# Performance work log

Hardware: AMD Instinct MI355X
Metric: run time of the kernel (lower is better)

Reference implementation:

```python
import jax, jax.numpy as jnp
import numpy as np

B, T, I, H, O = 256, 1024, 128, 256, 1

def setup_inputs() -> dict:
    key = jax.random.key(0)
    ks = jax.random.split(key, 7)
    s_ih = 1.0 / np.sqrt(H)
    return {
        "x": jax.random.normal(ks[0], (B, T, I), dtype=jnp.float32),
        "W_ih": jax.random.uniform(ks[1], (4 * H, I), minval=-s_ih, maxval=s_ih, dtype=jnp.float32),
        "W_hh": jax.random.uniform(ks[2], (4 * H, H), minval=-s_ih, maxval=s_ih, dtype=jnp.float32),
        "b_ih": jax.random.uniform(ks[3], (4 * H,), minval=-s_ih, maxval=s_ih, dtype=jnp.float32),
        "b_hh": jax.random.uniform(ks[4], (4 * H,), minval=-s_ih, maxval=s_ih, dtype=jnp.float32),
        "W_fc": jax.random.uniform(ks[5], (O, H), minval=-s_ih, maxval=s_ih, dtype=jnp.float32),
        "b_fc": jax.random.uniform(ks[6], (O,), minval=-s_ih, maxval=s_ih, dtype=jnp.float32),
    }

def _lstm_forward(x, W_ih, W_hh, b_ih, b_hh, W_fc, b_fc):
    # Precompute input projections for all timesteps in one big GEMM: [B,T,4H]
    x_proj = jnp.einsum('bti,gi->btg', x, W_ih) + b_ih + b_hh
    h0 = jnp.zeros((x.shape[0], W_hh.shape[1]), dtype=x.dtype)
    c0 = jnp.zeros_like(h0)
    Hd = W_hh.shape[1]

    def step(carry, xp_t):
        h, c = carry
        gates = xp_t + h @ W_hh.T  # [B, 4H]
        i_g = jax.nn.sigmoid(gates[:, 0 * Hd:1 * Hd])  # PyTorch gate order: i,f,g,o
        f_g = jax.nn.sigmoid(gates[:, 1 * Hd:2 * Hd])
        g_g = jnp.tanh(gates[:, 2 * Hd:3 * Hd])
        o_g = jax.nn.sigmoid(gates[:, 3 * Hd:4 * Hd])
        c_new = f_g * c + i_g * g_g
        h_new = o_g * jnp.tanh(c_new)
        return (h_new, c_new), None

    (h_T, _), _ = jax.lax.scan(step, (h0, c0), jnp.swapaxes(x_proj, 0, 1))
    return h_T @ W_fc.T + b_fc  # [B, O]

def reference(x, W_ih, W_hh, b_ih, b_hh, W_fc, b_fc):
    return _lstm_forward(x, W_ih, W_hh, b_ih, b_hh, W_fc, b_fc)
```

## Files before the change

### kernel.cpp

```cpp
#include <hip/hip_runtime.h>
#include <stdint.h>
#include <math.h>


typedef __attribute__((ext_vector_type(8))) __bf16 bf16x8;
typedef __attribute__((ext_vector_type(4))) float f32x4;
typedef __attribute__((ext_vector_type(4))) unsigned int u32x4;
typedef unsigned short u16;
typedef unsigned int u32;
typedef unsigned long long u64;

#define BK  16
#define JP  32
#define TT  1024
#define HD  256
#define ID  128

__device__ __forceinline__ u16 f2bf(float f) {
  u32 u = __float_as_uint(f);
  u += 0x7FFFu + ((u >> 16) & 1u);
  return (u16)(u >> 16);
}
__device__ __forceinline__ float bf2f(u16 h) { return __uint_as_float((u32)h << 16); }
__device__ __forceinline__ f32x4 mfma(bf16x8 a, bf16x8 b, f32x4 c) {
  return __builtin_amdgcn_mfma_f32_16x16x32_bf16(a, b, c, 0, 0, 0);
}
__device__ __forceinline__ float sigf(float x) {
  return __builtin_amdgcn_rcpf(1.f + __expf(-x));
}
__device__ __forceinline__ float tanhfast(float x) {
  float e = __expf(2.f * x);
  return 1.f - 2.f * __builtin_amdgcn_rcpf(e + 1.f);
}

__global__ __launch_bounds__(512, 2) void lstm_pk(
    const float* __restrict__ x, const float* __restrict__ Wih,
    const float* __restrict__ Whh, const float* __restrict__ bih,
    const float* __restrict__ bhh, const float* __restrict__ Wfc,
    const float* __restrict__ bfc, float* __restrict__ out,
    u16* __restrict__ hg)
{
  __shared__ u16 hHi[16][264], hLo[16][264];
  __shared__ u16 xHI[2][16][136], xLO[2][16][136];
  __shared__ u16 hS[2][2][16][40];
  __shared__ float red[8][16];

  const int tid  = threadIdx.x;
  const int bb   = blockIdx.x & 15, cb = blockIdx.x >> 4;
  const int b0   = bb * BK;
  const int lane = tid & 63, wave = tid >> 6;
  const int q    = lane >> 4, bcol = lane & 15;
  const int koff = q * 8;
  const int r15  = lane & 15;
  const int grow = (r15 & 3) * HD + cb * JP + wave * 4 + (r15 >> 2);
  const int jloc = wave * 4 + q;

  bf16x8 ahh_h[8], ahh_l[8], aih_h[4], aih_l[4];
#pragma unroll
  for (int kk = 0; kk < 8; ++kk) {
    const float* s = Whh + (size_t)grow * HD + kk * 32 + koff;
    float4 w0 = *(const float4*)(s), w1 = *(const float4*)(s + 4);
    float w[8] = {w0.x, w0.y, w0.z, w0.w, w1.x, w1.y, w1.z, w1.w};
    union { bf16x8 v; u16 u[8]; } th, tl;
#pragma unroll
    for (int e = 0; e < 8; ++e) {
      u16 hi = f2bf(w[e]); th.u[e] = hi; tl.u[e] = f2bf(w[e] - bf2f(hi));
    }
    ahh_h[kk] = th.v; ahh_l[kk] = tl.v;
  }
#pragma unroll
  for (int kk = 0; kk < 4; ++kk) {
    const float* s = Wih + (size_t)grow * ID + kk * 32 + koff;
    float4 w0 = *(const float4*)(s), w1 = *(const float4*)(s + 4);
    float w[8] = {w0.x, w0.y, w0.z, w0.w, w1.x, w1.y, w1.z, w1.w};
    union { bf16x8 v; u16 u[8]; } th, tl;
#pragma unroll
    for (int e = 0; e < 8; ++e) {
      u16 hi = f2bf(w[e]); th.u[e] = hi; tl.u[e] = f2bf(w[e] - bf2f(hi));
    }
    aih_h[kk] = th.v; aih_l[kk] = tl.v;
  }
  float biasr[4];
#pragma unroll
  for (int r = 0; r < 4; ++r) {
    int gr = r * HD + cb * JP + jloc;
    biasr[r] = bih[gr] + bhh[gr];
  }

  const int lb = tid >> 5;
  const int lc = (tid & 31) * 8;
  const u16* pH0 = hg + (((u32)(0 * 256 + b0 + lb)) << 8) + lc;
  const u16* pL0 = hg + (((u32)(1 * 256 + b0 + lb)) << 8) + lc;
  const u16* pH1 = hg + (((u32)(2 * 256 + b0 + lb)) << 8) + lc;
  const u16* pL1 = hg + (((u32)(3 * 256 + b0 + lb)) << 8) + lc;

  {
    int bi = tid >> 5, e4 = (tid & 31) * 4;
    float4 v = *(const float4*)(x + ((size_t)(b0 + bi) * TT) * ID + e4);
    float vf[4] = {v.x, v.y, v.z, v.w};
#pragma unroll
    for (int qq = 0; qq < 2; ++qq) {
      u16 h0 = f2bf(vf[2 * qq]),            h1 = f2bf(vf[2 * qq + 1]);
      u16 l0 = f2bf(vf[2 * qq] - bf2f(h0)), l1 = f2bf(vf[2 * qq + 1] - bf2f(h1));
      *(u32*)&xHI[0][bi][e4 + 2 * qq] = (u32)h0 | ((u32)h1 << 16);
      *(u32*)&xLO[0][bi][e4 + 2 * qq] = (u32)l0 | ((u32)l1 << 16);
    }
  }
  __syncthreads();

  float c_reg = 0.f, h_last = 0.f;

  for (int t = 0; t < TT; ++t) {
    const int p = t & 1, pn = p ^ 1;
    const u32 tag  = (u32)t & 3u;
    const u32 pat  = (tag & 1u) | ((tag >> 1) << 16);
    const u32 tagn = (u32)(t + 1) & 3u;
    const u16* aH = p ? pH1 : pH0;
    const u16* aL = p ? pL1 : pL0;

    u32x4 f0, f1;
    asm volatile("global_load_dwordx4 %0, %2, off sc0 sc1\n\t"
                 "global_load_dwordx4 %1, %3, off sc0 sc1"
                 : "=v"(f0), "=v"(f1) : "v"(aH), "v"(aL));

    f32x4 a0 = {0, 0, 0, 0}, a1 = {0, 0, 0, 0}, a2 = {0, 0, 0, 0};
#pragma unroll
    for (int kk = 0; kk < 4; ++kk) {
      bf16x8 bh = *(const bf16x8*)&xHI[p][bcol][kk * 32 + koff];
      bf16x8 bl = *(const bf16x8*)&xLO[p][bcol][kk * 32 + koff];
      a0 = mfma(aih_h[kk], bh, a0);
      a1 = mfma(aih_h[kk], bl, a1);
      a2 = mfma(aih_l[kk], bh, a2);
    }

    for (;;) {
      asm volatile("s_waitcnt vmcnt(0)" : "+v"(f0), "+v"(f1));
      u32 ok = (u32)((f0[0] & 0x10001u) == pat) & (u32)((f0[2] & 0x10001u) == pat)
             & (u32)((f1[0] & 0x10001u) == pat) & (u32)((f1[2] & 0x10001u) == pat);
      if (__all((int)ok)) break;
      __builtin_amdgcn_s_sleep(1);
      asm volatile("global_load_dwordx4 %0, %2, off sc0 sc1\n\t"
                   "global_load_dwordx4 %1, %3, off sc0 sc1\n\t"
                   "s_waitcnt vmcnt(0)"
                   : "=v"(f0), "=v"(f1) : "v"(aH), "v"(aL) : "memory");
    }

    float4 xv;
    if (t + 1 < TT)
      xv = *(const float4*)(x + ((size_t)(b0 + (tid >> 5)) * TT + (t + 1)) * ID + (tid & 31) * 4);

    *(u32x4*)&hHi[lb][lc] = f0;
    *(u32x4*)&hLo[lb][lc] = f1;
    __syncthreads();

#pragma unroll
    for (int kk = 0; kk < 8; ++kk) {
      bf16x8 bh = *(const bf16x8*)&hHi[bcol][kk * 32 + koff];
      bf16x8 bl = *(const bf16x8*)&hLo[bcol][kk * 32 + koff];
      a0 = mfma(ahh_h[kk], bh, a0);
      a1 = mfma(ahh_h[kk], bl, a1);
      a2 = mfma(ahh_l[kk], bh, a2);
    }

    {
      float g0 = a0[0] + a1[0] + a2[0] + biasr[0];
      float g1 = a0[1] + a1[1] + a2[1] + biasr[1];
      float g2 = a0[2] + a1[2] + a2[2] + biasr[2];
      float g3 = a0[3] + a1[3] + a2[3] + biasr[3];
      float ig = sigf(g0), fg = sigf(g1), gg = tanhfast(g2), og = sigf(g3);
      c_reg = fg * c_reg + ig * gg;
      float hn = og * tanhfast(c_reg);
      h_last = hn;
      u32 hi = f2bf(hn);
      if (q == 0) hi = (hi & ~1u) | (tagn & 1u);
      if (q == 1) hi = (hi & ~1u) | ((tagn >> 1) & 1u);
      u16 hi16 = (u16)hi;
      u32 lo = f2bf(hn - bf2f(hi16));
      if (q == 0) lo = (lo & ~1u) | (tagn & 1u);
      if (q == 1) lo = (lo & ~1u) | ((tagn >> 1) & 1u);
      hS[0][p][bcol][jloc] = hi16;
      hS[1][p][bcol][jloc] = (u16)lo;
    }

    if (t + 1 < TT) {
      float vf[4] = {xv.x, xv.y, xv.z, xv.w};
      int bi = tid >> 5, e4 = (tid & 31) * 4;
#pragma unroll
      for (int qq = 0; qq < 2; ++qq) {
        u16 h0 = f2bf(vf[2 * qq]),            h1 = f2bf(vf[2 * qq + 1]);
        u16 l0 = f2bf(vf[2 * qq] - bf2f(h0)), l1 = f2bf(vf[2 * qq + 1] - bf2f(h1));
        *(u32*)&xHI[pn][bi][e4 + 2 * qq] = (u32)h0 | ((u32)h1 << 16);
        *(u32*)&xLO[pn][bi][e4 + 2 * qq] = (u32)l0 | ((u32)l1 << 16);
      }
    }
    __syncthreads();

    if (tid >= 256) {
      int t2 = tid - 256, a = t2 >> 7, rem = t2 & 127, b = rem >> 3, ch = rem & 7;
      u64 v = *(const u64*)&hS[a][p][b][ch * 4];
      const u16* dst = hg + (((u32)((pn * 2 + a) * 256 + b0 + b)) << 8)
                          + (u32)(cb * JP + ch * 4);
      asm volatile("global_store_dwordx2 %0, %1, off sc0 sc1"
                   :: "v"(dst), "v"(v) : "memory");
    }
  }

  {
    float v = h_last * Wfc[cb * JP + jloc];
    v += __shfl_xor(v, 16);
    v += __shfl_xor(v, 32);
    if (lane < 16) red[wave][lane] = v;
  }
  __syncthreads();
  if (tid < 16) {
    float s = 0.f;
#pragma unroll
    for (int w = 0; w < 8; ++w) s += red[w][tid];
    if (cb == 0) s += bfc[0];
    atomicAdd(&out[b0 + tid], s);
  }
}

extern "C" void kernel_launch(void* const* d_in, const int* in_sizes, int n_in,
                              void* d_out, int out_size, void* d_ws, size_t ws_size,
                              hipStream_t stream) {
  const float* x   = (const float*)d_in[0];
  const float* Wih = (const float*)d_in[1];
  const float* Whh = (const float*)d_in[2];
  const float* bih = (const float*)d_in[3];
  const float* bhh = (const float*)d_in[4];
  const float* Wfc = (const float*)d_in[5];
  const float* bfc = (const float*)d_in[6];
  float* out = (float*)d_out;

  u16* hg = (u16*)d_ws;
  const size_t need = 4ull * 256 * 256 * sizeof(u16);

  hipMemsetAsync(d_ws, 0, need, stream);
  hipMemsetAsync(d_out, 0, (size_t)out_size * sizeof(float), stream);
  lstm_pk<<<128, 512, 0, stream>>>(x, Wih, Whh, bih, bhh, Wfc, bfc, out, hg);
}
```

Measured before the change: 2.736 ms.

## Interleave two batch groups per block to hide cross-block h exchange latency

Each block now handles two 16-row batch groups, A and B, over the same 32 hidden columns, and the grid is halved to 64 blocks. While group A's h-state poll and compute run, group B's global loads are already in flight, and the reverse. The aim is to overlap the inter-block synchronisation latency that dominates each timestep. Hi and lo bf16 halves are packed into one u32 per element and published directly per thread with a single store, replacing the shared staging area and the separate store phase. The risk is that half as many blocks leaves much of the GPU idle, and per-step serial work per block doubles.

```diff
diff --git a/kernel.cpp b/kernel.cpp
--- a/kernel.cpp
+++ b/kernel.cpp
@@ -8,9 +8,7 @@
 typedef __attribute__((ext_vector_type(4))) unsigned int u32x4;
 typedef unsigned short u16;
 typedef unsigned int u32;
-typedef unsigned long long u64;
-
-#define BK  16
+
 #define JP  32
 #define TT  1024
 #define HD  256
@@ -33,21 +31,20 @@
   return 1.f - 2.f * __builtin_amdgcn_rcpf(e + 1.f);
 }
 
-__global__ __launch_bounds__(512, 2) void lstm_pk(
+__global__ __launch_bounds__(512, 1) void lstm_pk(
     const float* __restrict__ x, const float* __restrict__ Wih,
     const float* __restrict__ Whh, const float* __restrict__ bih,
     const float* __restrict__ bhh, const float* __restrict__ Wfc,
     const float* __restrict__ bfc, float* __restrict__ out,
-    u16* __restrict__ hg)
+    u32* __restrict__ hg)
 {
-  __shared__ u16 hHi[16][264], hLo[16][264];
-  __shared__ u16 xHI[2][16][136], xLO[2][16][136];
-  __shared__ u16 hS[2][2][16][40];
+  __shared__ u16 hHi[2][16][264], hLo[2][16][264];
+  __shared__ u16 xHI[2][2][16][136], xLO[2][2][16][136];
   __shared__ float red[8][16];
 
   const int tid  = threadIdx.x;
-  const int bb   = blockIdx.x & 15, cb = blockIdx.x >> 4;
-  const int b0   = bb * BK;
+  const int pid  = blockIdx.x & 7, cb = blockIdx.x >> 3;
+  const int b0A  = pid * 16, b0B = (pid + 8) * 16;
   const int lane = tid & 63, wave = tid >> 6;
   const int q    = lane >> 4, bcol = lane & 15;
   const int koff = q * 8;
@@ -86,129 +83,167 @@
     int gr = r * HD + cb * JP + jloc;
     biasr[r] = bih[gr] + bhh[gr];
   }
-
-  const int lb = tid >> 5;
-  const int lc = (tid & 31) * 8;
-  const u16* pH0 = hg + (((u32)(0 * 256 + b0 + lb)) << 8) + lc;
-  const u16* pL0 = hg + (((u32)(1 * 256 + b0 + lb)) << 8) + lc;
-  const u16* pH1 = hg + (((u32)(2 * 256 + b0 + lb)) << 8) + lc;
-  const u16* pL1 = hg + (((u32)(3 * 256 + b0 + lb)) << 8) + lc;
-
-  {
-    int bi = tid >> 5, e4 = (tid & 31) * 4;
-    float4 v = *(const float4*)(x + ((size_t)(b0 + bi) * TT) * ID + e4);
-    float vf[4] = {v.x, v.y, v.z, v.w};
-#pragma unroll
-    for (int qq = 0; qq < 2; ++qq) {
-      u16 h0 = f2bf(vf[2 * qq]),            h1 = f2bf(vf[2 * qq + 1]);
-      u16 l0 = f2bf(vf[2 * qq] - bf2f(h0)), l1 = f2bf(vf[2 * qq + 1] - bf2f(h1));
-      *(u32*)&xHI[0][bi][e4 + 2 * qq] = (u32)h0 | ((u32)h1 << 16);
-      *(u32*)&xLO[0][bi][e4 + 2 * qq] = (u32)l0 | ((u32)l1 << 16);
-    }
-  }
-  __syncthreads();
-
-  float c_reg = 0.f, h_last = 0.f;
-
-  for (int t = 0; t < TT; ++t) {
-    const int p = t & 1, pn = p ^ 1;
-    const u32 tag  = (u32)t & 3u;
-    const u32 pat  = (tag & 1u) | ((tag >> 1) << 16);
-    const u32 tagn = (u32)(t + 1) & 3u;
-    const u16* aH = p ? pH1 : pH0;
-    const u16* aL = p ? pL1 : pL0;
-
-    u32x4 f0, f1;
+  float wfc = Wfc[cb * JP + jloc];
+  float bf0 = bfc[0];
+
+  const int lb = tid >> 5, lc = (tid & 31) * 8;
+  const u32* ldA0 = hg +           (b0A + lb) * 256 + lc;
+  const u32* ldA1 = hg + 65536 +   (b0A + lb) * 256 + lc;
+  const u32* ldB0 = hg +           (b0B + lb) * 256 + lc;
+  const u32* ldB1 = hg + 65536 +   (b0B + lb) * 256 + lc;
+  u32* pbA0 = hg +         (b0A + bcol) * 256 + cb * JP + jloc;
+  u32* pbA1 = pbA0 + 65536;
+  u32* pbB0 = hg +         (b0B + bcol) * 256 + cb * JP + jloc;
+  u32* pbB1 = pbB0 + 65536;
+  const float* xbA = x + (size_t)(b0A + lb) * TT * ID + (tid & 31) * 4;
+  const float* xbB = x + (size_t)(b0B + lb) * TT * ID + (tid & 31) * 4;
+
+  auto issue2 = [&](u32x4& g0, u32x4& g1, const u32* ap) {
     asm volatile("global_load_dwordx4 %0, %2, off sc0 sc1\n\t"
-                 "global_load_dwordx4 %1, %3, off sc0 sc1"
-                 : "=v"(f0), "=v"(f1) : "v"(aH), "v"(aL));
-
-    f32x4 a0 = {0, 0, 0, 0}, a1 = {0, 0, 0, 0}, a2 = {0, 0, 0, 0};
+                 "global_load_dwordx4 %1, %2, off offset:16 sc0 sc1"
+                 : "=v"(g0), "=v"(g1) : "v"(ap));
+  };
+  auto loadx = [&](f32x4& v, const float* ap) {
+    asm volatile("global_load_dwordx4 %0, %1, off" : "=v"(v) : "v"(ap));
+  };
+  auto pubst = [&](u32* ap, u32 w) {
+    asm volatile("global_store_dword %0, %1, off sc0 sc1" :: "v"(ap), "v"(w) : "memory");
+  };
+  auto xproj = [&](int g, int buf, f32x4& a0, f32x4& a1, f32x4& a2) {
 #pragma unroll
     for (int kk = 0; kk < 4; ++kk) {
-      bf16x8 bh = *(const bf16x8*)&xHI[p][bcol][kk * 32 + koff];
-      bf16x8 bl = *(const bf16x8*)&xLO[p][bcol][kk * 32 + koff];
+      bf16x8 bh = *(const bf16x8*)&xHI[g][buf][bcol][kk * 32 + koff];
+      bf16x8 bl = *(const bf16x8*)&xLO[g][buf][bcol][kk * 32 + koff];
       a0 = mfma(aih_h[kk], bh, a0);
       a1 = mfma(aih_h[kk], bl, a1);
       a2 = mfma(aih_l[kk], bh, a2);
     }
-
-    for (;;) {
-      asm volatile("s_waitcnt vmcnt(0)" : "+v"(f0), "+v"(f1));
-      u32 ok = (u32)((f0[0] & 0x10001u) == pat) & (u32)((f0[2] & 0x10001u) == pat)
-             & (u32)((f1[0] & 0x10001u) == pat) & (u32)((f1[2] & 0x10001u) == pat);
-      if (__all((int)ok)) break;
-      __builtin_amdgcn_s_sleep(1);
-      asm volatile("global_load_dwordx4 %0, %2, off sc0 sc1\n\t"
-                   "global_load_dwordx4 %1, %3, off sc0 sc1\n\t"
-                   "s_waitcnt vmcnt(0)"
-                   : "=v"(f0), "=v"(f1) : "v"(aH), "v"(aL) : "memory");
-    }
-
-    float4 xv;
-    if (t + 1 < TT)
-      xv = *(const float4*)(x + ((size_t)(b0 + (tid >> 5)) * TT + (t + 1)) * ID + (tid & 31) * 4);
-
-    *(u32x4*)&hHi[lb][lc] = f0;
-    *(u32x4*)&hLo[lb][lc] = f1;
-    __syncthreads();
-
+  };
+  auto hproj = [&](int g, f32x4& a0, f32x4& a1, f32x4& a2) {
 #pragma unroll
     for (int kk = 0; kk < 8; ++kk) {
-      bf16x8 bh = *(const bf16x8*)&hHi[bcol][kk * 32 + koff];
-      bf16x8 bl = *(const bf16x8*)&hLo[bcol][kk * 32 + koff];
+      bf16x8 bh = *(const bf16x8*)&hHi[g][bcol][kk * 32 + koff];
+      bf16x8 bl = *(const bf16x8*)&hLo[g][bcol][kk * 32 + koff];
       a0 = mfma(ahh_h[kk], bh, a0);
       a1 = mfma(ahh_h[kk], bl, a1);
       a2 = mfma(ahh_l[kk], bh, a2);
     }
-
-    {
-      float g0 = a0[0] + a1[0] + a2[0] + biasr[0];
-      float g1 = a0[1] + a1[1] + a2[1] + biasr[1];
-      float g2 = a0[2] + a1[2] + a2[2] + biasr[2];
-      float g3 = a0[3] + a1[3] + a2[3] + biasr[3];
-      float ig = sigf(g0), fg = sigf(g1), gg = tanhfast(g2), og = sigf(g3);
-      c_reg = fg * c_reg + ig * gg;
-      float hn = og * tanhfast(c_reg);
-      h_last = hn;
-      u32 hi = f2bf(hn);
-      if (q == 0) hi = (hi & ~1u) | (tagn & 1u);
-      if (q == 1) hi = (hi & ~1u) | ((tagn >> 1) & 1u);
-      u16 hi16 = (u16)hi;
-      u32 lo = f2bf(hn - bf2f(hi16));
-      if (q == 0) lo = (lo & ~1u) | (tagn & 1u);
-      if (q == 1) lo = (lo & ~1u) | ((tagn >> 1) & 1u);
-      hS[0][p][bcol][jloc] = hi16;
-      hS[1][p][bcol][jloc] = (u16)lo;
-    }
-
-    if (t + 1 < TT) {
-      float vf[4] = {xv.x, xv.y, xv.z, xv.w};
-      int bi = tid >> 5, e4 = (tid & 31) * 4;
-#pragma unroll
-      for (int qq = 0; qq < 2; ++qq) {
-        u16 h0 = f2bf(vf[2 * qq]),            h1 = f2bf(vf[2 * qq + 1]);
-        u16 l0 = f2bf(vf[2 * qq] - bf2f(h0)), l1 = f2bf(vf[2 * qq + 1] - bf2f(h1));
-        *(u32*)&xHI[pn][bi][e4 + 2 * qq] = (u32)h0 | ((u32)h1 << 16);
-        *(u32*)&xLO[pn][bi][e4 + 2 * qq] = (u32)l0 | ((u32)l1 << 16);
-      }
-    }
+  };
+  auto stageH = [&](int g, u32x4 f0, u32x4 f1) {
+    u32x4 hv = {(f0[0] & 0xFFFFu) | (f0[1] << 16), (f0[2] & 0xFFFFu) | (f0[3] << 16),
+                (f1[0] & 0xFFFFu) | (f1[1] << 16), (f1[2] & 0xFFFFu) | (f1[3] << 16)};
+    u32x4 lv = {(f0[0] >> 16) | (f0[1] & 0xFFFF0000u), (f0[2] >> 16) | (f0[3] & 0xFFFF0000u),
+                (f1[0] >> 16) | (f1[1] & 0xFFFF0000u), (f1[2] >> 16) | (f1[3] & 0xFFFF0000u)};
+    *(u32x4*)&hHi[g][lb][lc] = hv;
+    *(u32x4*)&hLo[g][lb][lc] = lv;
+  };
+  auto xstage = [&](int g, int buf, f32x4 v) {
+    int bi = tid >> 5, e4 = (tid & 31) * 4;
+#pragma unroll
+    for (int qq = 0; qq < 2; ++qq) {
+      float v0 = v[2 * qq], v1 = v[2 * qq + 1];
+      u16 h0 = f2bf(v0), h1 = f2bf(v1);
+      u16 l0 = f2bf(v0 - bf2f(h0)), l1 = f2bf(v1 - bf2f(h1));
+      *(u32*)&xHI[g][buf][bi][e4 + 2 * qq] = (u32)h0 | ((u32)h1 << 16);
+      *(u32*)&xLO[g][buf][bi][e4 + 2 * qq] = (u32)l0 | ((u32)l1 << 16);
+    }
+  };
+  auto cell = [&](f32x4 a0, f32x4 a1, f32x4 a2, float& c, float& hl,
+                  u32 t1, u32* pp) {
+    float g0 = a0[0] + a1[0] + a2[0] + biasr[0];
+    float g1 = a0[1] + a1[1] + a2[1] + biasr[1];
+    float g2 = a0[2] + a1[2] + a2[2] + biasr[2];
+    float g3 = a0[3] + a1[3] + a2[3] + biasr[3];
+    float ig = sigf(g0), fg = sigf(g1), gg = tanhfast(g2), og = sigf(g3);
+    c = fg * c + ig * gg;
+    float hn = og * tanhfast(c);
+    hl = hn;
+    u32 hi = (f2bf(hn) & ~1u) | (t1 & 1u);
+    float res = hn - bf2f((u16)hi);
+    u32 lo = (f2bf(res) & ~1u) | ((t1 >> 1) & 1u);
+    pubst(pp, (hi & 0xFFFFu) | (lo << 16));
+  };
+
+  {
+    f32x4 vA = *(const f32x4*)xbA;
+    f32x4 vB = *(const f32x4*)xbB;
+    xstage(0, 0, vA);
+    xstage(1, 0, vB);
+  }
+  asm volatile("s_waitcnt vmcnt(0) lgkmcnt(0)" ::: "memory");
+  u32x4 fA0, fA1, fB0, fB1;
+  issue2(fA0, fA1, ldA0);
+  __syncthreads();
+
+  float cA = 0.f, cB = 0.f, hlA = 0.f, hlB = 0.f;
+  f32x4 xvA, xvB;
+
+  for (int t = 0; t < TT; ++t) {
+    const int p = t & 1, pn = p ^ 1;
+    const u32 pat  = ((u32)t & 1u) | ((((u32)t >> 1) & 1u) << 16);
+    const u32 t1   = (u32)t + 1u;
+    const int tn   = (t + 1 < TT) ? (t + 1) : (TT - 1);
+
+    f32x4 a0 = {0,0,0,0}, a1 = {0,0,0,0}, a2 = {0,0,0,0};
+    xproj(0, p, a0, a1, a2);
+    if (t == 0) asm volatile("s_waitcnt vmcnt(0)"
+                             : "+v"(fA0), "+v"(fA1), "+v"(a0), "+v"(a1), "+v"(a2));
+    else        asm volatile("s_waitcnt vmcnt(1)"
+                             : "+v"(fA0), "+v"(fA1), "+v"(a0), "+v"(a1), "+v"(a2));
+    for (;;) {
+      u32 ok = 1;
+#pragma unroll
+      for (int w = 0; w < 4; ++w) ok &= (u32)((fA0[w] & 0x10001u) == pat);
+#pragma unroll
+      for (int w = 0; w < 4; ++w) ok &= (u32)((fA1[w] & 0x10001u) == pat);
+      if (__all((int)ok)) break;
+      __builtin_amdgcn_s_sleep(1);
+      const u32* ap = p ? ldA1 : ldA0;
+      asm volatile("global_load_dwordx4 %0, %2, off sc0 sc1\n\t"
+                   "global_load_dwordx4 %1, %2, off offset:16 sc0 sc1\n\t"
+                   "s_waitcnt vmcnt(0)"
+                   : "=v"(fA0), "=v"(fA1) : "v"(ap) : "memory");
+    }
+    stageH(0, fA0, fA1);
+    issue2(fB0, fB1, p ? ldB1 : ldB0);
+    loadx(xvA, xbA + (size_t)tn * ID);
     __syncthreads();
-
-    if (tid >= 256) {
-      int t2 = tid - 256, a = t2 >> 7, rem = t2 & 127, b = rem >> 3, ch = rem & 7;
-      u64 v = *(const u64*)&hS[a][p][b][ch * 4];
-      const u16* dst = hg + (((u32)((pn * 2 + a) * 256 + b0 + b)) << 8)
-                          + (u32)(cb * JP + ch * 4);
-      asm volatile("global_store_dwordx2 %0, %1, off sc0 sc1"
-                   :: "v"(dst), "v"(v) : "memory");
-    }
+    hproj(0, a0, a1, a2);
+    cell(a0, a1, a2, cA, hlA, t1, pn ? pbA1 : pbA0);
+    asm volatile("s_waitcnt vmcnt(1)" : "+v"(xvA));
+    xstage(0, pn, xvA);
+
+    f32x4 b0 = {0,0,0,0}, b1 = {0,0,0,0}, b2 = {0,0,0,0};
+    xproj(1, p, b0, b1, b2);
+    asm volatile("s_waitcnt vmcnt(1)"
+                 : "+v"(fB0), "+v"(fB1), "+v"(b0), "+v"(b1), "+v"(b2));
+    for (;;) {
+      u32 ok = 1;
+#pragma unroll
+      for (int w = 0; w < 4; ++w) ok &= (u32)((fB0[w] & 0x10001u) == pat);
+#pragma unroll
+      for (int w = 0; w < 4; ++w) ok &= (u32)((fB1[w] & 0x10001u) == pat);
+      if (__all((int)ok)) break;
+      __builtin_amdgcn_s_sleep(1);
+      const u32* ap = p ? ldB1 : ldB0;
+      asm volatile("global_load_dwordx4 %0, %2, off sc0 sc1\n\t"
+                   "global_load_dwordx4 %1, %2, off offset:16 sc0 sc1\n\t"
+                   "s_waitcnt vmcnt(0)"
+                   : "=v"(fB0), "=v"(fB1) : "v"(ap) : "memory");
+    }
+    stageH(1, fB0, fB1);
+    issue2(fA0, fA1, pn ? ldA1 : ldA0);
+    loadx(xvB, xbB + (size_t)tn * ID);
+    __syncthreads();
+    hproj(1, b0, b1, b2);
+    cell(b0, b1, b2, cB, hlB, t1, pn ? pbB1 : pbB0);
+    asm volatile("s_waitcnt vmcnt(1)" : "+v"(xvB));
+    xstage(1, pn, xvB);
   }
 
   {
-    float v = h_last * Wfc[cb * JP + jloc];
-    v += __shfl_xor(v, 16);
-    v += __shfl_xor(v, 32);
+    float v = hlA * wfc;
+    v += __shfl_xor(v, 16); v += __shfl_xor(v, 32);
     if (lane < 16) red[wave][lane] = v;
   }
   __syncthreads();
@@ -216,8 +251,22 @@
     float s = 0.f;
 #pragma unroll
     for (int w = 0; w < 8; ++w) s += red[w][tid];
-    if (cb == 0) s += bfc[0];
-    atomicAdd(&out[b0 + tid], s);
+    if (cb == 0) s += bf0;
+    atomicAdd(&out[b0A + tid], s);
+  }
+  __syncthreads();
+  {
+    float v = hlB * wfc;
+    v += __shfl_xor(v, 16); v += __shfl_xor(v, 32);
+    if (lane < 16) red[wave][lane] = v;
+  }
+  __syncthreads();
+  if (tid < 16) {
+    float s = 0.f;
+#pragma unroll
+    for (int w = 0; w < 8; ++w) s += red[w][tid];
+    if (cb == 0) s += bf0;
+    atomicAdd(&out[b0B + tid], s);
   }
 }
 
@@ -233,10 +282,10 @@
   const float* bfc = (const float*)d_in[6];
   float* out = (float*)d_out;
 
-  u16* hg = (u16*)d_ws;
-  const size_t need = 4ull * 256 * 256 * sizeof(u16);
+  u32* hg = (u32*)d_ws;
+  const size_t need = 2ull * 256 * 256 * sizeof(u32);
 
   hipMemsetAsync(d_ws, 0, need, stream);
   hipMemsetAsync(d_out, 0, (size_t)out_size * sizeof(float), stream);
-  lstm_pk<<<128, 512, 0, stream>>>(x, Wih, Whh, bih, bhh, Wfc, bfc, out, hg);
-}
+  lstm_pk<<<64, 512, 0, stream>>>(x, Wih, Whh, bih, bhh, Wfc, bfc, out, hg);
+}
```

New measurement: 4.223 ms. 54.4% more time.
